# Kernel tuning notes

Measured on AMD Instinct MI355X. Metric: run time of the kernel, lower is better.

Reference implementation:

```python
import math
import jax, jax.numpy as jnp
import numpy as np

S, H, D = 2048, 16, 128

def setup_inputs() -> dict:
    key = jax.random.key(0)
    kq, kk, kv = jax.random.split(key, 3)
    Q = jax.random.normal(kq, (S, H, D), dtype=jnp.float32)
    K = jax.random.normal(kk, (S, H, D), dtype=jnp.float32)
    V = jax.random.normal(kv, (S, H, D), dtype=jnp.float32)
    return {"Q": Q, "K": K, "V": V}

def reference(Q, K, V):
    s, h, d = Q.shape
    # scores[i,h,j] = sum_d Q[i,h,d] * K[j,h,d]  (torch einsum 'ijk,kjl->ijl' with K.T)
    scores = jnp.einsum('ihd,jhd->ihj', Q, K) / np.float32(math.sqrt(d))
    # causal mask: y -= triu(inf, 1) broadcast over heads -> -inf above diagonal
    causal = jnp.triu(jnp.ones((s, s), dtype=bool), k=1)  # [S, S]
    scores = jnp.where(causal[:, None, :], -jnp.inf, scores)
    attn = jax.nn.softmax(scores, axis=2)  # softmax over keys (dim 2)
    # out[i,h,d] = sum_j attn[i,h,j] * V[j,h,d]
    return jnp.einsum('ihj,jhd->ihd', attn, V)
```

## Files before the change

kernel.cpp:

```cpp
#include <hip/hip_runtime.h>
#include <hip/hip_bf16.h>

#define S_LEN 2048
#define NH 16
#define HD 128
#define KBLK 64
#define SM_BOUND 14.0f

typedef short short8 __attribute__((ext_vector_type(8)));
typedef float f32x4 __attribute__((ext_vector_type(4)));

__device__ __forceinline__ ushort f2bf(float f) {
  union { float f; unsigned u; } v; v.f = f;
  unsigned u = v.u;
  return (ushort)((u + 0x7fffu + ((u >> 16) & 1u)) >> 16);
}

#define GLDS(gp, lp)                                                      \
  __builtin_amdgcn_global_load_lds(                                       \
      (const __attribute__((address_space(1))) void*)(gp),                \
      (__attribute__((address_space(3))) void*)(lp), 16, 0, 0)

__global__ __launch_bounds__(256)
void prep(const float* __restrict__ Kg, const float* __restrict__ Vg,
          ushort* __restrict__ Kb, ushort* __restrict__ Vb) {
  __shared__ ushort lt[64 * HD];
  const int tid = threadIdx.x;
  const int h = blockIdx.x & 15;
  const int j0 = (blockIdx.x >> 4) * 64;

#pragma unroll
  for (int it = 0; it < 8; ++it) {
    int flat = it * 256 + tid;
    int r = flat >> 5, d4 = (flat & 31) * 4;
    float4 v = *(const float4*)(Kg + ((size_t)(j0 + r) * NH + h) * HD + d4);
    ushort4 b;
    b.x = f2bf(v.x); b.y = f2bf(v.y); b.z = f2bf(v.z); b.w = f2bf(v.w);
    *(ushort4*)(Kb + ((size_t)h * S_LEN + j0 + r) * HD + d4) = b;
  }
#pragma unroll
  for (int it = 0; it < 8; ++it) {
    int flat = it * 256 + tid;
    int r = flat >> 5, d4 = (flat & 31) * 4;
    float4 v = *(const float4*)(Vg + ((size_t)(j0 + r) * NH + h) * HD + d4);
    ushort4 b;
    b.x = f2bf(v.x); b.y = f2bf(v.y); b.z = f2bf(v.z); b.w = f2bf(v.w);
    *(ushort4*)(&lt[r * 128 + (d4 ^ ((r & 7) << 3))]) = b;
  }
  __syncthreads();
  const int d = tid >> 1, half = tid & 1;
  ushort vals[32];
#pragma unroll
  for (int j = 0; j < 32; ++j) {
    int jjj = half * 32 + j;
    vals[j] = lt[jjj * 128 + (d ^ ((jjj & 7) << 3))];
  }
  ushort* dst = Vb + ((size_t)h * HD + d) * S_LEN + j0 + half * 32;
#pragma unroll
  for (int q = 0; q < 4; ++q) {
    short8 w;
#pragma unroll
    for (int e = 0; e < 8; ++e) w[e] = (short)vals[q * 8 + e];
    *(short8*)(dst + q * 8) = w;
  }
}

__global__ __launch_bounds__(512, 2)
void attn_fwd6(const float* __restrict__ Qg, const ushort* __restrict__ Kb,
               const ushort* __restrict__ Vb, float* __restrict__ Og) {
  __shared__ ushort lds_k[3][KBLK * HD];
  __shared__ ushort lds_vt[3][HD * KBLK];
  __shared__ ushort lds_p[64 * 64];
  __shared__ float  lsc[2][4][2][16];

  const int tid = threadIdx.x;
  const int l   = tid & 63;
  const int wv  = tid >> 6;
  const int qf  = wv >> 2;
  const int kh  = wv & 3;
  const int dh  = wv & 3;
  const int lr  = l & 15;
  const int lg  = l >> 4;

  const int bid = blockIdx.x;
  const int h   = bid & 15;
  const int jj  = bid >> 4;
  const int qtA = 31 - jj;
  const int qbA = qtA * 64, qbB = jj * 64;

  const ushort* khp = Kb + (size_t)h * S_LEN * HD;
  const ushort* vhp = Vb + (size_t)h * HD * S_LEN;

  const int b0 = tid, b1 = 512 + tid;
  const int r0 = b0 >> 4, r1 = b1 >> 4;
  const int koff0 = r0 * 128 + (((b0 & 15) ^ (r0 & 7)) << 3);
  const int koff1 = r1 * 128 + (((b1 & 15) ^ (r1 & 7)) << 3);
  const int dd0 = b0 >> 3, dd1 = b1 >> 3;
  const int voff0 = dd0 * S_LEN + (((b0 & 7) ^ (dd0 & 7)) << 3);
  const int voff1 = dd1 * S_LEN + (((b1 & 7) ^ (dd1 & 7)) << 3);

  auto stage = [&](int buf, int kc) {
    const ushort* kbase = khp + (size_t)kc * (KBLK * HD);
    GLDS(kbase + koff0, &lds_k[buf][tid * 8]);
    GLDS(kbase + koff1, &lds_k[buf][4096 + tid * 8]);
    const ushort* vbase = vhp + (size_t)kc * KBLK;
    GLDS(vbase + voff0, &lds_vt[buf][tid * 8]);
    GLDS(vbase + voff1, &lds_vt[buf][4096 + tid * 8]);
  };

  const float scale = 0.08838834764831845f;
  short8 qfrA[2][4], qfrB[2][4];
  auto loadQ = [&](short8 (&dst)[2][4], int qb) {
#pragma unroll
    for (int qc = 0; qc < 2; ++qc) {
      const float* qsrc = Qg + ((size_t)(qb + qf * 32 + qc * 16 + lr) * NH + h) * HD;
#pragma unroll
      for (int dk = 0; dk < 4; ++dk) {
        float4 a = *(const float4*)(qsrc + dk * 32 + lg * 8);
        float4 b2 = *(const float4*)(qsrc + dk * 32 + lg * 8 + 4);
        short8 f;
        f[0] = (short)f2bf(a.x * scale);  f[1] = (short)f2bf(a.y * scale);
        f[2] = (short)f2bf(a.z * scale);  f[3] = (short)f2bf(a.w * scale);
        f[4] = (short)f2bf(b2.x * scale); f[5] = (short)f2bf(b2.y * scale);
        f[6] = (short)f2bf(b2.z * scale); f[7] = (short)f2bf(b2.w * scale);
        dst[qc][dk] = f;
      }
    }
  };
  loadQ(qfrA, qbA);
  loadQ(qfrB, qbB);

  f32x4 oacc[2][2];
#pragma unroll
  for (int qc = 0; qc < 2; ++qc)
#pragma unroll
    for (int dt = 0; dt < 2; ++dt) oacc[qc][dt] = (f32x4){0.f, 0.f, 0.f, 0.f};
  float l_run[2] = {0.f, 0.f};

  auto epilogue = [&](int qb) {
    float t0 = l_run[0], t1 = l_run[1];
    t0 += __shfl_xor(t0, 16, 64); t0 += __shfl_xor(t0, 32, 64);
    t1 += __shfl_xor(t1, 16, 64); t1 += __shfl_xor(t1, 32, 64);
    if (lg == 0) { lsc[qf][kh][0][lr] = t0; lsc[qf][kh][1][lr] = t1; }
    __syncthreads();
    float inv[2][4];
#pragma unroll
    for (int qc = 0; qc < 2; ++qc)
#pragma unroll
      for (int i = 0; i < 4; ++i) {
        int q15 = lg * 4 + i;
        float sl = (lsc[qf][0][qc][q15] + lsc[qf][1][qc][q15]) +
                   (lsc[qf][2][qc][q15] + lsc[qf][3][qc][q15]);
        inv[qc][i] = 1.0f / sl;
      }
#pragma unroll
    for (int qc = 0; qc < 2; ++qc)
#pragma unroll
      for (int dt = 0; dt < 2; ++dt)
#pragma unroll
        for (int i = 0; i < 4; ++i) {
          int qg = qb + qf * 32 + qc * 16 + lg * 4 + i;
          Og[((size_t)qg * NH + h) * HD + dh * 32 + dt * 16 + lr] =
              oacc[qc][dt][i] * inv[qc][i];
        }
  };

  stage(0, 0);
  stage(1, 1);

  for (int g = 0; g < 33; ++g) {
    if (g == 32) { asm volatile("s_waitcnt vmcnt(0)" ::: "memory"); }
    else         { asm volatile("s_waitcnt vmcnt(4)" ::: "memory"); }
    asm volatile("s_barrier" ::: "memory");
    if (g + 2 < 33) {
      int t = g + 2;
      stage(t % 3, (t <= qtA) ? t : (t - qtA - 1));
    }
    const int bI = g % 3;
    const ushort* lk = lds_k[bI];
    const ushort* lv = lds_vt[bI];
    const bool tB = (g > qtA);
    const int kc = tB ? (g - qtA - 1) : g;
    const int qb = tB ? qbB : qbA;

    f32x4 s0 = (f32x4){0.f, 0.f, 0.f, 0.f};
    f32x4 s1 = (f32x4){0.f, 0.f, 0.f, 0.f};
    const int krow = kh * 16 + lr;
    __builtin_amdgcn_s_setprio(1);
    if (!tB) {
#pragma unroll
      for (int dk = 0; dk < 4; ++dk) {
        short8 kf = *(const short8*)&lk[krow * 128 + ((dk * 32 + lg * 8) ^ ((lr & 7) << 3))];
        s0 = __builtin_amdgcn_mfma_f32_16x16x32_bf16(kf, qfrA[0][dk], s0, 0, 0, 0);
        s1 = __builtin_amdgcn_mfma_f32_16x16x32_bf16(kf, qfrA[1][dk], s1, 0, 0, 0);
      }
    } else {
#pragma unroll
      for (int dk = 0; dk < 4; ++dk) {
        short8 kf = *(const short8*)&lk[krow * 128 + ((dk * 32 + lg * 8) ^ ((lr & 7) << 3))];
        s0 = __builtin_amdgcn_mfma_f32_16x16x32_bf16(kf, qfrB[0][dk], s0, 0, 0, 0);
        s1 = __builtin_amdgcn_mfma_f32_16x16x32_bf16(kf, qfrB[1][dk], s1, 0, 0, 0);
      }
    }
    __builtin_amdgcn_s_setprio(0);

    float p0[4], p1[4];
    if (g == qtA || g == 32) {
      const int qg0 = qb + qf * 32 + lr;
#pragma unroll
      for (int i = 0; i < 4; ++i) {
        int kg = kc * 64 + kh * 16 + lg * 4 + i;
        float e0 = __expf(s0[i] - SM_BOUND);
        float e1 = __expf(s1[i] - SM_BOUND);
        p0[i] = (kg > qg0) ? 0.f : e0;
        p1[i] = (kg > qg0 + 16) ? 0.f : e1;
      }
    } else {
#pragma unroll
      for (int i = 0; i < 4; ++i) {
        p0[i] = __expf(s0[i] - SM_BOUND);
        p1[i] = __expf(s1[i] - SM_BOUND);
      }
    }
    l_run[0] += (p0[0] + p0[1]) + (p0[2] + p0[3]);
    l_run[1] += (p1[0] + p1[1]) + (p1[2] + p1[3]);

    {
      int q0 = qf * 32 + lr;
      int q1 = q0 + 16;
      unsigned w;
      asm("v_cvt_pk_bf16_f32 %0, %1, %2" : "=v"(w) : "v"(p0[0]), "v"(p0[1]));
      *(unsigned*)&lds_p[q0 * 64 + ((kh * 16 + lg * 4 + 0) ^ ((q0 & 7) << 3))] = w;
      asm("v_cvt_pk_bf16_f32 %0, %1, %2" : "=v"(w) : "v"(p0[2]), "v"(p0[3]));
      *(unsigned*)&lds_p[q0 * 64 + ((kh * 16 + lg * 4 + 2) ^ ((q0 & 7) << 3))] = w;
      asm("v_cvt_pk_bf16_f32 %0, %1, %2" : "=v"(w) : "v"(p1[0]), "v"(p1[1]));
      *(unsigned*)&lds_p[q1 * 64 + ((kh * 16 + lg * 4 + 0) ^ ((q1 & 7) << 3))] = w;
      asm("v_cvt_pk_bf16_f32 %0, %1, %2" : "=v"(w) : "v"(p1[2]), "v"(p1[3]));
      *(unsigned*)&lds_p[q1 * 64 + ((kh * 16 + lg * 4 + 2) ^ ((q1 & 7) << 3))] = w;
    }
    asm volatile("s_waitcnt lgkmcnt(0)" ::: "memory");
    asm volatile("s_barrier" ::: "memory");
    __builtin_amdgcn_sched_barrier(0);

    short8 pa0[2], pa1[2];
    {
      int q0 = qf * 32 + lr;
      int q1 = q0 + 16;
      pa0[0] = *(const short8*)&lds_p[q0 * 64 + ((lg * 8) ^ ((q0 & 7) << 3))];
      pa0[1] = *(const short8*)&lds_p[q0 * 64 + ((32 + lg * 8) ^ ((q0 & 7) << 3))];
      pa1[0] = *(const short8*)&lds_p[q1 * 64 + ((lg * 8) ^ ((q1 & 7) << 3))];
      pa1[1] = *(const short8*)&lds_p[q1 * 64 + ((32 + lg * 8) ^ ((q1 & 7) << 3))];
    }
    __builtin_amdgcn_s_setprio(1);
#pragma unroll
    for (int dt = 0; dt < 2; ++dt) {
      int d = dh * 32 + dt * 16 + lr;
#pragma unroll
      for (int ks = 0; ks < 2; ++ks) {
        short8 vf = *(const short8*)&lv[d * 64 + ((ks * 32 + lg * 8) ^ ((d & 7) << 3))];
        oacc[0][dt] = __builtin_amdgcn_mfma_f32_16x16x32_bf16(pa0[ks], vf, oacc[0][dt], 0, 0, 0);
        oacc[1][dt] = __builtin_amdgcn_mfma_f32_16x16x32_bf16(pa1[ks], vf, oacc[1][dt], 0, 0, 0);
      }
    }
    __builtin_amdgcn_s_setprio(0);

    if (g == qtA) {
      epilogue(qbA);
#pragma unroll
      for (int qc = 0; qc < 2; ++qc)
#pragma unroll
        for (int dt = 0; dt < 2; ++dt) oacc[qc][dt] = (f32x4){0.f, 0.f, 0.f, 0.f};
      l_run[0] = 0.f; l_run[1] = 0.f;
    }
  }
  epilogue(qbB);
}

__global__ __launch_bounds__(256, 2)
void attn_fwd_fb(const float* __restrict__ Qg, const float* __restrict__ Kg,
                 const float* __restrict__ Vg, float* __restrict__ Og) {
  __shared__ ushort lds_k[KBLK * HD];
  __shared__ ushort lds_vt[HD * KBLK];
  __shared__ ushort lds_p[4][16 * KBLK];

  const int tid = threadIdx.x;
  const int l  = tid & 63;
  const int wv = tid >> 6;
  const int lr = l & 15;
  const int lg = l >> 4;

  const int bid = blockIdx.x;
  const int h  = bid & 15;
  const int qi = bid >> 4;
  const int qt = (qi < 16) ? (31 - 2 * qi) : (2 * (qi - 16));
  const int qbase = qt * 64;

  short8 qf[4];
  {
    const float* qsrc = Qg + ((size_t)(qbase + wv * 16 + lr) * NH + h) * HD;
#pragma unroll
    for (int dk = 0; dk < 4; ++dk) {
      float4 a = *(const float4*)(qsrc + dk * 32 + lg * 8);
      float4 b = *(const float4*)(qsrc + dk * 32 + lg * 8 + 4);
      short8 f;
      f[0] = (short)f2bf(a.x); f[1] = (short)f2bf(a.y);
      f[2] = (short)f2bf(a.z); f[3] = (short)f2bf(a.w);
      f[4] = (short)f2bf(b.x); f[5] = (short)f2bf(b.y);
      f[6] = (short)f2bf(b.z); f[7] = (short)f2bf(b.w);
      qf[dk] = f;
    }
  }

  f32x4 oacc[8];
#pragma unroll
  for (int dt = 0; dt < 8; ++dt) oacc[dt] = (f32x4){0.f, 0.f, 0.f, 0.f};
  float l_run[4] = {0.f, 0.f, 0.f, 0.f};

  const float scale = 0.08838834764831845f;
  const int nch = qt + 1;

  for (int c = 0; c < nch; ++c) {
    const int k0 = c * KBLK;
    __syncthreads();
#pragma unroll
    for (int it = 0; it < 8; ++it) {
      int flat = (it * 256 + tid) * 4;
      int r = flat >> 7, d = flat & 127;
      float4 v = *(const float4*)(Kg + ((size_t)(k0 + r) * NH + h) * HD + d);
      int idx = (r * 128 + d) ^ ((r & 7) << 3);
      ushort4 b4;
      b4.x = f2bf(v.x); b4.y = f2bf(v.y); b4.z = f2bf(v.z); b4.w = f2bf(v.w);
      *(ushort4*)&lds_k[idx] = b4;
    }
#pragma unroll
    for (int it = 0; it < 8; ++it) {
      int d0 = wv * 32 + it * 4;
      float4 v = *(const float4*)(Vg + ((size_t)(k0 + l) * NH + h) * HD + d0);
      lds_vt[((d0 + 0) * 64 + l) ^ (((d0 + 0) & 7) << 3)] = f2bf(v.x);
      lds_vt[((d0 + 1) * 64 + l) ^ (((d0 + 1) & 7) << 3)] = f2bf(v.y);
      lds_vt[((d0 + 2) * 64 + l) ^ (((d0 + 2) & 7) << 3)] = f2bf(v.z);
      lds_vt[((d0 + 3) * 64 + l) ^ (((d0 + 3) & 7) << 3)] = f2bf(v.w);
    }
    __syncthreads();

    f32x4 sacc[4];
#pragma unroll
    for (int kc = 0; kc < 4; ++kc) {
      sacc[kc] = (f32x4){0.f, 0.f, 0.f, 0.f};
#pragma unroll
      for (int dk = 0; dk < 4; ++dk) {
        int row = kc * 16 + lr;
        int idx = (row * 128 + dk * 32 + lg * 8) ^ ((row & 7) << 3);
        short8 kf = *(const short8*)&lds_k[idx];
        sacc[kc] = __builtin_amdgcn_mfma_f32_16x16x32_bf16(qf[dk], kf, sacc[kc], 0, 0, 0);
      }
    }

    float p[4][4];
    if (c == qt) {
#pragma unroll
      for (int i = 0; i < 4; ++i) {
        int qg = qbase + wv * 16 + lg * 4 + i;
#pragma unroll
        for (int kc = 0; kc < 4; ++kc) {
          float e = __expf(sacc[kc][i] * scale - SM_BOUND);
          p[kc][i] = (k0 + kc * 16 + lr > qg) ? 0.f : e;
        }
      }
    } else {
#pragma unroll
      for (int i = 0; i < 4; ++i)
#pragma unroll
        for (int kc = 0; kc < 4; ++kc)
          p[kc][i] = __expf(sacc[kc][i] * scale - SM_BOUND);
    }
#pragma unroll
    for (int i = 0; i < 4; ++i)
      l_run[i] += (p[0][i] + p[1][i]) + (p[2][i] + p[3][i]);

#pragma unroll
    for (int kc = 0; kc < 4; ++kc)
#pragma unroll
      for (int i = 0; i < 4; ++i) {
        int row = lg * 4 + i, col = kc * 16 + lr;
        lds_p[wv][(row * 64 + col) ^ ((row & 7) << 3)] = f2bf(p[kc][i]);
      }
    asm volatile("s_waitcnt lgkmcnt(0)" ::: "memory");
    __builtin_amdgcn_sched_barrier(0);

    short8 pa[2];
#pragma unroll
    for (int ks = 0; ks < 2; ++ks) {
      int idx = (lr * 64 + ks * 32 + lg * 8) ^ ((lr & 7) << 3);
      pa[ks] = *(const short8*)&lds_p[wv][idx];
    }

#pragma unroll
    for (int dt = 0; dt < 8; ++dt) {
#pragma unroll
      for (int ks = 0; ks < 2; ++ks) {
        int d = dt * 16 + lr;
        int idx = (d * 64 + ks * 32 + lg * 8) ^ ((d & 7) << 3);
        short8 vf = *(const short8*)&lds_vt[idx];
        oacc[dt] = __builtin_amdgcn_mfma_f32_16x16x32_bf16(pa[ks], vf, oacc[dt], 0, 0, 0);
      }
    }
  }

#pragma unroll
  for (int mk = 1; mk <= 8; mk <<= 1)
#pragma unroll
    for (int i = 0; i < 4; ++i)
      l_run[i] += __shfl_xor(l_run[i], mk, 64);
  float inv[4];
#pragma unroll
  for (int i = 0; i < 4; ++i) inv[i] = 1.0f / l_run[i];
#pragma unroll
  for (int dt = 0; dt < 8; ++dt)
#pragma unroll
    for (int i = 0; i < 4; ++i) {
      int qg = qbase + wv * 16 + lg * 4 + i;
      Og[((size_t)qg * NH + h) * HD + dt * 16 + lr] = oacc[dt][i] * inv[i];
    }
}

extern "C" void kernel_launch(void* const* d_in, const int* in_sizes, int n_in,
                              void* d_out, int out_size, void* d_ws, size_t ws_size,
                              hipStream_t stream) {
  (void)in_sizes; (void)n_in; (void)out_size;
  const float* Q = (const float*)d_in[0];
  const float* K = (const float*)d_in[1];
  const float* V = (const float*)d_in[2];
  float* O = (float*)d_out;

  const size_t elems = (size_t)S_LEN * NH * HD;
  const size_t need = 2 * elems * sizeof(ushort);
  if (ws_size >= need) {
    ushort* Kb = (ushort*)d_ws;
    ushort* Vb = Kb + elems;
    prep<<<dim3(512), dim3(256), 0, stream>>>(K, V, Kb, Vb);
    attn_fwd6<<<dim3(256), dim3(512), 0, stream>>>(Q, Kb, Vb, O);
  } else {
    attn_fwd_fb<<<dim3(512), dim3(256), 0, stream>>>(Q, K, V, O);
  }
}
```

Before: 64.36 us.

## Compute transposed S=K·Q^T so P stays in registers for PV MFMA

Adds an attention kernel that computes scores transposed (K rows times Q), so each lane's exp'd probabilities can feed a 16x16x16 bf16 MFMA for the PV product directly from registers. This avoids staging P through LDS. Each wave now covers a key slice with all 128 output dims. Partial output accumulators are then reduced across the four key-split waves in LDS during the epilogue, which adds barriers and more accumulator registers. The old kernel is kept as a fallback when the 16x16x16 MFMA builtin is unavailable.

```diff
diff --git a/kernel.cpp b/kernel.cpp
--- a/kernel.cpp
+++ b/kernel.cpp
@@ -8,7 +8,15 @@
 #define SM_BOUND 14.0f
 
 typedef short short8 __attribute__((ext_vector_type(8)));
+typedef short short4v __attribute__((ext_vector_type(4)));
 typedef float f32x4 __attribute__((ext_vector_type(4)));
+
+#if __has_builtin(__builtin_amdgcn_mfma_f32_16x16x16bf16_1k)
+#define HAVE_MFMA16 1
+#define MFMA16(a, b, c) __builtin_amdgcn_mfma_f32_16x16x16bf16_1k(a, b, c, 0, 0, 0)
+#else
+#define HAVE_MFMA16 0
+#endif
 
 __device__ __forceinline__ ushort f2bf(float f) {
   union { float f; unsigned u; } v; v.f = f;
@@ -65,8 +73,239 @@
   }
 }
 
+#if HAVE_MFMA16
 __global__ __launch_bounds__(512, 2)
-void attn_fwd6(const float* __restrict__ Qg, const ushort* __restrict__ Kb,
+void attn_main(const float* __restrict__ Qg, const ushort* __restrict__ Kb,
+               const ushort* __restrict__ Vb, float* __restrict__ Og) {
+  __shared__ ushort lds_k[3][KBLK * HD];
+  __shared__ ushort lds_vt[3][HD * KBLK];
+  __shared__ float  osc[2][4096];
+  __shared__ float  lsc[2][4][2][16];
+
+  const int tid = threadIdx.x;
+  const int l   = tid & 63;
+  const int wv  = tid >> 6;
+  const int qf  = wv >> 2;
+  const int kh  = wv & 3;
+  const int lr  = l & 15;
+  const int lg  = l >> 4;
+
+  const int bid = blockIdx.x;
+  const int h   = bid & 15;
+  const int jj  = bid >> 4;
+  const int qtA = 31 - jj;
+  const int qbA = qtA * 64, qbB = jj * 64;
+
+  const ushort* khp = Kb + (size_t)h * S_LEN * HD;
+  const ushort* vhp = Vb + (size_t)h * HD * S_LEN;
+
+  const int b0 = tid, b1 = 512 + tid;
+  const int r0 = b0 >> 4, r1 = b1 >> 4;
+  const int koff0 = r0 * 128 + (((b0 & 15) ^ (r0 & 7)) << 3);
+  const int koff1 = r1 * 128 + (((b1 & 15) ^ (r1 & 7)) << 3);
+  const int dd0 = b0 >> 3, dd1 = b1 >> 3;
+  const int voff0 = dd0 * S_LEN + (((b0 & 7) ^ (dd0 & 7)) << 3);
+  const int voff1 = dd1 * S_LEN + (((b1 & 7) ^ (dd1 & 7)) << 3);
+
+  auto stage = [&](int buf, int kc) {
+    const ushort* kbase = khp + (size_t)kc * (KBLK * HD);
+    GLDS(kbase + koff0, &lds_k[buf][tid * 8]);
+    GLDS(kbase + koff1, &lds_k[buf][4096 + tid * 8]);
+    const ushort* vbase = vhp + (size_t)kc * KBLK;
+    GLDS(vbase + voff0, &lds_vt[buf][tid * 8]);
+    GLDS(vbase + voff1, &lds_vt[buf][4096 + tid * 8]);
+  };
+
+  const float scale = 0.08838834764831845f;
+  short8 qfrA[2][4], qfrB[2][4];
+  auto loadQ = [&](short8 (&dst)[2][4], int qb) {
+#pragma unroll
+    for (int qc = 0; qc < 2; ++qc) {
+      const float* qsrc = Qg + ((size_t)(qb + qf * 32 + qc * 16 + lr) * NH + h) * HD;
+#pragma unroll
+      for (int dk = 0; dk < 4; ++dk) {
+        float4 a = *(const float4*)(qsrc + dk * 32 + lg * 8);
+        float4 b2 = *(const float4*)(qsrc + dk * 32 + lg * 8 + 4);
+        short8 f;
+        f[0] = (short)f2bf(a.x * scale);  f[1] = (short)f2bf(a.y * scale);
+        f[2] = (short)f2bf(a.z * scale);  f[3] = (short)f2bf(a.w * scale);
+        f[4] = (short)f2bf(b2.x * scale); f[5] = (short)f2bf(b2.y * scale);
+        f[6] = (short)f2bf(b2.z * scale); f[7] = (short)f2bf(b2.w * scale);
+        dst[qc][dk] = f;
+      }
+    }
+  };
+  loadQ(qfrA, qbA);
+  loadQ(qfrB, qbB);
+
+  f32x4 oaccT[2][8];
+#pragma unroll
+  for (int qc = 0; qc < 2; ++qc)
+#pragma unroll
+    for (int dt = 0; dt < 8; ++dt) oaccT[qc][dt] = (f32x4){0.f, 0.f, 0.f, 0.f};
+  float l_run[2] = {0.f, 0.f};
+
+  auto epilogue = [&](int qb) {
+    float t0 = l_run[0], t1 = l_run[1];
+    t0 += __shfl_xor(t0, 16, 64); t0 += __shfl_xor(t0, 32, 64);
+    t1 += __shfl_xor(t1, 16, 64); t1 += __shfl_xor(t1, 32, 64);
+    if (lg == 0) { lsc[qf][kh][0][lr] = t0; lsc[qf][kh][1][lr] = t1; }
+    if (kh == 0) {
+#pragma unroll
+      for (int qc = 0; qc < 2; ++qc)
+#pragma unroll
+        for (int dt = 0; dt < 8; ++dt) {
+          int q = qc * 16 + lr;
+          int du = (((dt * 4 + lg) ^ (q & 7)) << 2);
+          *(f32x4*)&osc[qf][q * 128 + du] = oaccT[qc][dt];
+        }
+    }
+    __syncthreads();
+    if (kh == 1) {
+#pragma unroll
+      for (int qc = 0; qc < 2; ++qc)
+#pragma unroll
+        for (int dt = 0; dt < 8; ++dt) {
+          int q = qc * 16 + lr;
+          int du = (((dt * 4 + lg) ^ (q & 7)) << 2);
+          f32x4 v = *(const f32x4*)&osc[qf][q * 128 + du];
+          v += oaccT[qc][dt];
+          *(f32x4*)&osc[qf][q * 128 + du] = v;
+        }
+    }
+    __syncthreads();
+    if (kh == 2) {
+#pragma unroll
+      for (int qc = 0; qc < 2; ++qc)
+#pragma unroll
+        for (int dt = 0; dt < 8; ++dt) {
+          int q = qc * 16 + lr;
+          int du = (((dt * 4 + lg) ^ (q & 7)) << 2);
+          f32x4 v = *(const f32x4*)&osc[qf][q * 128 + du];
+          v += oaccT[qc][dt];
+          *(f32x4*)&osc[qf][q * 128 + du] = v;
+        }
+    }
+    __syncthreads();
+    if (kh == 3) {
+      float inv[2];
+#pragma unroll
+      for (int qc = 0; qc < 2; ++qc)
+        inv[qc] = 1.0f / ((lsc[qf][0][qc][lr] + lsc[qf][1][qc][lr]) +
+                          (lsc[qf][2][qc][lr] + lsc[qf][3][qc][lr]));
+#pragma unroll
+      for (int qc = 0; qc < 2; ++qc)
+#pragma unroll
+        for (int dt = 0; dt < 8; ++dt) {
+          int q = qc * 16 + lr;
+          int du = (((dt * 4 + lg) ^ (q & 7)) << 2);
+          f32x4 v = *(const f32x4*)&osc[qf][q * 128 + du];
+          v += oaccT[qc][dt];
+          int qg = qb + qf * 32 + q;
+          float4 o;
+          o.x = v[0] * inv[qc]; o.y = v[1] * inv[qc];
+          o.z = v[2] * inv[qc]; o.w = v[3] * inv[qc];
+          *(float4*)(Og + ((size_t)qg * NH + h) * HD + dt * 16 + lg * 4) = o;
+        }
+    }
+  };
+
+  stage(0, 0);
+  stage(1, 1);
+
+  for (int g = 0; g < 33; ++g) {
+    if (g == 32) { asm volatile("s_waitcnt vmcnt(0)" ::: "memory"); }
+    else         { asm volatile("s_waitcnt vmcnt(4)" ::: "memory"); }
+    asm volatile("s_barrier" ::: "memory");
+    if (g + 2 < 33) {
+      int t = g + 2;
+      stage(t % 3, (t <= qtA) ? t : (t - qtA - 1));
+    }
+    const int bI = g % 3;
+    const ushort* lk = lds_k[bI];
+    const ushort* lv = lds_vt[bI];
+    const bool tB = (g > qtA);
+    const int kc = tB ? (g - qtA - 1) : g;
+    const int qb = tB ? qbB : qbA;
+
+    f32x4 s0 = (f32x4){0.f, 0.f, 0.f, 0.f};
+    f32x4 s1 = (f32x4){0.f, 0.f, 0.f, 0.f};
+    const int krow = kh * 16 + lr;
+    __builtin_amdgcn_s_setprio(1);
+    if (!tB) {
+#pragma unroll
+      for (int dk = 0; dk < 4; ++dk) {
+        short8 kf = *(const short8*)&lk[krow * 128 + ((dk * 32 + lg * 8) ^ ((lr & 7) << 3))];
+        s0 = __builtin_amdgcn_mfma_f32_16x16x32_bf16(kf, qfrA[0][dk], s0, 0, 0, 0);
+        s1 = __builtin_amdgcn_mfma_f32_16x16x32_bf16(kf, qfrA[1][dk], s1, 0, 0, 0);
+      }
+    } else {
+#pragma unroll
+      for (int dk = 0; dk < 4; ++dk) {
+        short8 kf = *(const short8*)&lk[krow * 128 + ((dk * 32 + lg * 8) ^ ((lr & 7) << 3))];
+        s0 = __builtin_amdgcn_mfma_f32_16x16x32_bf16(kf, qfrB[0][dk], s0, 0, 0, 0);
+        s1 = __builtin_amdgcn_mfma_f32_16x16x32_bf16(kf, qfrB[1][dk], s1, 0, 0, 0);
+      }
+    }
+    __builtin_amdgcn_s_setprio(0);
+
+    float p0[4], p1[4];
+    if (g == qtA || g == 32) {
+      const int qg0 = qb + qf * 32 + lr;
+#pragma unroll
+      for (int i = 0; i < 4; ++i) {
+        int kg = kc * 64 + kh * 16 + lg * 4 + i;
+        float e0 = __expf(s0[i] - SM_BOUND);
+        float e1 = __expf(s1[i] - SM_BOUND);
+        p0[i] = (kg > qg0) ? 0.f : e0;
+        p1[i] = (kg > qg0 + 16) ? 0.f : e1;
+      }
+    } else {
+#pragma unroll
+      for (int i = 0; i < 4; ++i) {
+        p0[i] = __expf(s0[i] - SM_BOUND);
+        p1[i] = __expf(s1[i] - SM_BOUND);
+      }
+    }
+    l_run[0] += (p0[0] + p0[1]) + (p0[2] + p0[3]);
+    l_run[1] += (p1[0] + p1[1]) + (p1[2] + p1[3]);
+
+    short4v pb0, pb1;
+    {
+      union { unsigned u[2]; short4v v; } c0, c1;
+      asm("v_cvt_pk_bf16_f32 %0, %1, %2" : "=v"(c0.u[0]) : "v"(p0[0]), "v"(p0[1]));
+      asm("v_cvt_pk_bf16_f32 %0, %1, %2" : "=v"(c0.u[1]) : "v"(p0[2]), "v"(p0[3]));
+      asm("v_cvt_pk_bf16_f32 %0, %1, %2" : "=v"(c1.u[0]) : "v"(p1[0]), "v"(p1[1]));
+      asm("v_cvt_pk_bf16_f32 %0, %1, %2" : "=v"(c1.u[1]) : "v"(p1[2]), "v"(p1[3]));
+      pb0 = c0.v; pb1 = c1.v;
+    }
+
+    __builtin_amdgcn_s_setprio(1);
+#pragma unroll
+    for (int dt = 0; dt < 8; ++dt) {
+      int d = dt * 16 + lr;
+      short4v va = *(const short4v*)&lv[d * 64 + ((kh * 16 + lg * 4) ^ ((d & 7) << 3))];
+      oaccT[0][dt] = MFMA16(va, pb0, oaccT[0][dt]);
+      oaccT[1][dt] = MFMA16(va, pb1, oaccT[1][dt]);
+    }
+    __builtin_amdgcn_s_setprio(0);
+
+    if (g == qtA) {
+      epilogue(qbA);
+#pragma unroll
+      for (int qc = 0; qc < 2; ++qc)
+#pragma unroll
+        for (int dt = 0; dt < 8; ++dt) oaccT[qc][dt] = (f32x4){0.f, 0.f, 0.f, 0.f};
+      l_run[0] = 0.f; l_run[1] = 0.f;
+    }
+  }
+  epilogue(qbB);
+}
+
+#else
+
+__global__ __launch_bounds__(512, 2)
+void attn_main(const float* __restrict__ Qg, const ushort* __restrict__ Kb,
                const ushort* __restrict__ Vb, float* __restrict__ Og) {
   __shared__ ushort lds_k[3][KBLK * HD];
   __shared__ ushort lds_vt[3][HD * KBLK];
@@ -275,6 +514,7 @@
   }
   epilogue(qbB);
 }
+#endif
 
 __global__ __launch_bounds__(256, 2)
 void attn_fwd_fb(const float* __restrict__ Qg, const float* __restrict__ Kg,
@@ -439,7 +679,7 @@
     ushort* Kb = (ushort*)d_ws;
     ushort* Vb = Kb + elems;
     prep<<<dim3(512), dim3(256), 0, stream>>>(K, V, Kb, Vb);
-    attn_fwd6<<<dim3(256), dim3(512), 0, stream>>>(Q, Kb, Vb, O);
+    attn_main<<<dim3(256), dim3(512), 0, stream>>>(Q, Kb, Vb, O);
   } else {
     attn_fwd_fb<<<dim3(512), dim3(256), 0, stream>>>(Q, K, V, O);
   }
```

New measurement: 67.02 us. 4.1% more time.

## Split each paired causal attention block across two workgroups with partial-sum combine

Applied to the files above, without the earlier changes.

Replaces the single 256-block kernel, where each block processed a paired long and short query tile, with a 512-block kernel. Each pair of blocks splits the 33 key chunks about evenly (16 and 17): one block does half of the long tile, the other finishes it and also does the short tile. The long tile's partial outputs and row sums go to workspace and a new combine kernel merges them. Inside the kernel, P stays in registers and feeds 16x16x16 MFMAs with each wave covering all 128 head dimensions, dropping the P round-trip through LDS. The trade-off is a cross-wave LDS reduction in the epilogue, an extra kernel launch, more workspace traffic, and the fixed max-bound softmax is unchanged.

```diff
diff --git a/kernel.cpp b/kernel.cpp
--- a/kernel.cpp
+++ b/kernel.cpp
@@ -8,7 +8,11 @@
 #define SM_BOUND 14.0f
 
 typedef short short8 __attribute__((ext_vector_type(8)));
+typedef short short4v __attribute__((ext_vector_type(4)));
 typedef float f32x4 __attribute__((ext_vector_type(4)));
+
+#define MFMA32(a, b, c) __builtin_amdgcn_mfma_f32_16x16x32_bf16(a, b, c, 0, 0, 0)
+#define MFMA16(a, b, c) __builtin_amdgcn_mfma_f32_16x16x16bf16_1k(a, b, c, 0, 0, 0)
 
 __device__ __forceinline__ ushort f2bf(float f) {
   union { float f; unsigned u; } v; v.f = f;
@@ -65,12 +69,13 @@
   }
 }
 
-__global__ __launch_bounds__(512, 2)
-void attn_fwd6(const float* __restrict__ Qg, const ushort* __restrict__ Kb,
-               const ushort* __restrict__ Vb, float* __restrict__ Og) {
-  __shared__ ushort lds_k[3][KBLK * HD];
-  __shared__ ushort lds_vt[3][HD * KBLK];
-  __shared__ ushort lds_p[64 * 64];
+__global__ __launch_bounds__(512, 4)
+void attn_split2(const float* __restrict__ Qg, const ushort* __restrict__ Kb,
+                 const ushort* __restrict__ Vb, float* __restrict__ Og,
+                 float* __restrict__ Opart, float* __restrict__ lpart) {
+  __shared__ ushort lds_k[2][KBLK * HD];
+  __shared__ ushort lds_vt[2][HD * KBLK];
+  __shared__ float  osc[16 * 128];
   __shared__ float  lsc[2][4][2][16];
 
   const int tid = threadIdx.x;
@@ -78,39 +83,47 @@
   const int wv  = tid >> 6;
   const int qf  = wv >> 2;
   const int kh  = wv & 3;
-  const int dh  = wv & 3;
   const int lr  = l & 15;
   const int lg  = l >> 4;
 
   const int bid = blockIdx.x;
-  const int h   = bid & 15;
-  const int jj  = bid >> 4;
-  const int qtA = 31 - jj;
-  const int qbA = qtA * 64, qbB = jj * 64;
+  const int w    = bid >> 3;
+  const int h    = ((bid & 7) << 1) + (w >> 5);
+  const int r5v  = w & 31;
+  const int jj   = r5v >> 1;
+  const int role = r5v & 1;
+  const int qtA  = 31 - jj;
+  const int qbA  = qtA << 6, qbB = jj << 6;
+  const int pid  = h * 16 + jj;
+  const int nA   = role ? (16 - jj) : 16;
+  const int nch  = role ? 17 : 16;
+  const int kcA0 = role ? 16 : 0;
 
   const ushort* khp = Kb + (size_t)h * S_LEN * HD;
   const ushort* vhp = Vb + (size_t)h * HD * S_LEN;
 
-  const int b0 = tid, b1 = 512 + tid;
-  const int r0 = b0 >> 4, r1 = b1 >> 4;
-  const int koff0 = r0 * 128 + (((b0 & 15) ^ (r0 & 7)) << 3);
-  const int koff1 = r1 * 128 + (((b1 & 15) ^ (r1 & 7)) << 3);
-  const int dd0 = b0 >> 3, dd1 = b1 >> 3;
-  const int voff0 = dd0 * S_LEN + (((b0 & 7) ^ (dd0 & 7)) << 3);
-  const int voff1 = dd1 * S_LEN + (((b1 & 7) ^ (dd1 & 7)) << 3);
-
+  int koff[2], voff[2];
+#pragma unroll
+  for (int i = 0; i < 2; ++i) {
+    int Dg = i * 512 + tid;
+    int r = Dg >> 4, c = Dg & 15;
+    koff[i] = r * 128 + ((c ^ (r & 7)) << 3);
+    int d = Dg >> 3, gp = Dg & 7;
+    voff[i] = d * S_LEN + (((gp - (d & 7)) & 7) << 3);
+  }
   auto stage = [&](int buf, int kc) {
     const ushort* kbase = khp + (size_t)kc * (KBLK * HD);
-    GLDS(kbase + koff0, &lds_k[buf][tid * 8]);
-    GLDS(kbase + koff1, &lds_k[buf][4096 + tid * 8]);
+    GLDS(kbase + koff[0], &lds_k[buf][tid * 8]);
+    GLDS(kbase + koff[1], &lds_k[buf][4096 + tid * 8]);
     const ushort* vbase = vhp + (size_t)kc * KBLK;
-    GLDS(vbase + voff0, &lds_vt[buf][tid * 8]);
-    GLDS(vbase + voff1, &lds_vt[buf][4096 + tid * 8]);
+    GLDS(vbase + voff[0], &lds_vt[buf][tid * 8]);
+    GLDS(vbase + voff[1], &lds_vt[buf][4096 + tid * 8]);
   };
+  auto kc_of = [&](int g) { return (g < nA) ? (kcA0 + g) : (g - nA); };
 
   const float scale = 0.08838834764831845f;
-  short8 qfrA[2][4], qfrB[2][4];
-  auto loadQ = [&](short8 (&dst)[2][4], int qb) {
+  short8 qfr[2][4];
+  auto loadQ = [&](int qb) {
 #pragma unroll
     for (int qc = 0; qc < 2; ++qc) {
       const float* qsrc = Qg + ((size_t)(qb + qf * 32 + qc * 16 + lr) * NH + h) * HD;
@@ -123,89 +136,120 @@
         f[2] = (short)f2bf(a.z * scale);  f[3] = (short)f2bf(a.w * scale);
         f[4] = (short)f2bf(b2.x * scale); f[5] = (short)f2bf(b2.y * scale);
         f[6] = (short)f2bf(b2.z * scale); f[7] = (short)f2bf(b2.w * scale);
-        dst[qc][dk] = f;
+        qfr[qc][dk] = f;
       }
     }
   };
-  loadQ(qfrA, qbA);
-  loadQ(qfrB, qbB);
-
-  f32x4 oacc[2][2];
+  loadQ(qbA);
+
+  f32x4 oaccT[2][8];
 #pragma unroll
   for (int qc = 0; qc < 2; ++qc)
 #pragma unroll
-    for (int dt = 0; dt < 2; ++dt) oacc[qc][dt] = (f32x4){0.f, 0.f, 0.f, 0.f};
+    for (int dt = 0; dt < 8; ++dt) oaccT[qc][dt] = (f32x4){0.f, 0.f, 0.f, 0.f};
   float l_run[2] = {0.f, 0.f};
 
-  auto epilogue = [&](int qb) {
+  auto epilogue = [&](int mode, int qb, int slot) {
     float t0 = l_run[0], t1 = l_run[1];
     t0 += __shfl_xor(t0, 16, 64); t0 += __shfl_xor(t0, 32, 64);
     t1 += __shfl_xor(t1, 16, 64); t1 += __shfl_xor(t1, 32, 64);
     if (lg == 0) { lsc[qf][kh][0][lr] = t0; lsc[qf][kh][1][lr] = t1; }
-    __syncthreads();
-    float inv[2][4];
-#pragma unroll
-    for (int qc = 0; qc < 2; ++qc)
-#pragma unroll
-      for (int i = 0; i < 4; ++i) {
-        int q15 = lg * 4 + i;
-        float sl = (lsc[qf][0][qc][q15] + lsc[qf][1][qc][q15]) +
-                   (lsc[qf][2][qc][q15] + lsc[qf][3][qc][q15]);
-        inv[qc][i] = 1.0f / sl;
-      }
-#pragma unroll
-    for (int qc = 0; qc < 2; ++qc)
-#pragma unroll
-      for (int dt = 0; dt < 2; ++dt)
-#pragma unroll
-        for (int i = 0; i < 4; ++i) {
-          int qg = qb + qf * 32 + qc * 16 + lg * 4 + i;
-          Og[((size_t)qg * NH + h) * HD + dh * 32 + dt * 16 + lr] =
-              oacc[qc][dt][i] * inv[qc][i];
+    asm volatile("s_waitcnt lgkmcnt(0)" ::: "memory");
+    asm volatile("s_barrier" ::: "memory");
+    const size_t pid2 = (size_t)(pid * 2 + slot);
+#pragma unroll
+    for (int qfp = 0; qfp < 2; ++qfp)
+#pragma unroll
+      for (int qcp = 0; qcp < 2; ++qcp) {
+        if (qf == qfp && kh == 0) {
+#pragma unroll
+          for (int dt = 0; dt < 8; ++dt)
+            *(f32x4*)&osc[lr * 128 + (((dt * 4 + lg) ^ (lr & 7)) << 2)] = oaccT[qcp][dt];
         }
+        asm volatile("s_waitcnt lgkmcnt(0)" ::: "memory");
+        asm volatile("s_barrier" ::: "memory");
+        if (qf == qfp && kh == 1) {
+#pragma unroll
+          for (int dt = 0; dt < 8; ++dt) {
+            f32x4 v = *(const f32x4*)&osc[lr * 128 + (((dt * 4 + lg) ^ (lr & 7)) << 2)];
+            v += oaccT[qcp][dt];
+            *(f32x4*)&osc[lr * 128 + (((dt * 4 + lg) ^ (lr & 7)) << 2)] = v;
+          }
+        }
+        asm volatile("s_waitcnt lgkmcnt(0)" ::: "memory");
+        asm volatile("s_barrier" ::: "memory");
+        if (qf == qfp && kh == 2) {
+#pragma unroll
+          for (int dt = 0; dt < 8; ++dt) {
+            f32x4 v = *(const f32x4*)&osc[lr * 128 + (((dt * 4 + lg) ^ (lr & 7)) << 2)];
+            v += oaccT[qcp][dt];
+            *(f32x4*)&osc[lr * 128 + (((dt * 4 + lg) ^ (lr & 7)) << 2)] = v;
+          }
+        }
+        asm volatile("s_waitcnt lgkmcnt(0)" ::: "memory");
+        asm volatile("s_barrier" ::: "memory");
+        if (qf == qfp && kh == 3) {
+          float lsum = (lsc[qfp][0][qcp][lr] + lsc[qfp][1][qcp][lr]) +
+                       (lsc[qfp][2][qcp][lr] + lsc[qfp][3][qcp][lr]);
+          int qrow = qfp * 32 + qcp * 16 + lr;
+          if (mode == 0) {
+            if (lg == 0) lpart[pid2 * 64 + qrow] = lsum;
+            float* dst = Opart + pid2 * 8192 + (size_t)qrow * 128;
+#pragma unroll
+            for (int dt = 0; dt < 8; ++dt) {
+              f32x4 v = *(const f32x4*)&osc[lr * 128 + (((dt * 4 + lg) ^ (lr & 7)) << 2)];
+              v += oaccT[qcp][dt];
+              float4 o; o.x = v[0]; o.y = v[1]; o.z = v[2]; o.w = v[3];
+              *(float4*)(dst + dt * 16 + lg * 4) = o;
+            }
+          } else {
+            float inv = 1.0f / lsum;
+            int qg = qb + qrow;
+#pragma unroll
+            for (int dt = 0; dt < 8; ++dt) {
+              f32x4 v = *(const f32x4*)&osc[lr * 128 + (((dt * 4 + lg) ^ (lr & 7)) << 2)];
+              v += oaccT[qcp][dt];
+              float4 o;
+              o.x = v[0] * inv; o.y = v[1] * inv; o.z = v[2] * inv; o.w = v[3] * inv;
+              *(float4*)(Og + ((size_t)qg * NH + h) * HD + dt * 16 + lg * 4) = o;
+            }
+          }
+        }
+        asm volatile("s_waitcnt lgkmcnt(0)" ::: "memory");
+        asm volatile("s_barrier" ::: "memory");
+      }
   };
 
-  stage(0, 0);
-  stage(1, 1);
-
-  for (int g = 0; g < 33; ++g) {
-    if (g == 32) { asm volatile("s_waitcnt vmcnt(0)" ::: "memory"); }
-    else         { asm volatile("s_waitcnt vmcnt(4)" ::: "memory"); }
+  stage(0, kc_of(0));
+  stage(1, kc_of(1));
+
+  for (int g = 0; g < nch; ++g) {
+    if (g + 1 < nch) { asm volatile("s_waitcnt vmcnt(4)" ::: "memory"); }
+    else             { asm volatile("s_waitcnt vmcnt(0)" ::: "memory"); }
     asm volatile("s_barrier" ::: "memory");
-    if (g + 2 < 33) {
-      int t = g + 2;
-      stage(t % 3, (t <= qtA) ? t : (t - qtA - 1));
-    }
-    const int bI = g % 3;
-    const ushort* lk = lds_k[bI];
-    const ushort* lv = lds_vt[bI];
-    const bool tB = (g > qtA);
-    const int kc = tB ? (g - qtA - 1) : g;
+
+    const int b = g & 1;
+    const ushort* lk = lds_k[b];
+    const ushort* lv = lds_vt[b];
+    const bool tB = (g >= nA);
+    const int kc = kc_of(g);
     const int qb = tB ? qbB : qbA;
+    const bool diag = ((kc << 6) == qb);
 
     f32x4 s0 = (f32x4){0.f, 0.f, 0.f, 0.f};
     f32x4 s1 = (f32x4){0.f, 0.f, 0.f, 0.f};
     const int krow = kh * 16 + lr;
     __builtin_amdgcn_s_setprio(1);
-    if (!tB) {
-#pragma unroll
-      for (int dk = 0; dk < 4; ++dk) {
-        short8 kf = *(const short8*)&lk[krow * 128 + ((dk * 32 + lg * 8) ^ ((lr & 7) << 3))];
-        s0 = __builtin_amdgcn_mfma_f32_16x16x32_bf16(kf, qfrA[0][dk], s0, 0, 0, 0);
-        s1 = __builtin_amdgcn_mfma_f32_16x16x32_bf16(kf, qfrA[1][dk], s1, 0, 0, 0);
-      }
-    } else {
-#pragma unroll
-      for (int dk = 0; dk < 4; ++dk) {
-        short8 kf = *(const short8*)&lk[krow * 128 + ((dk * 32 + lg * 8) ^ ((lr & 7) << 3))];
-        s0 = __builtin_amdgcn_mfma_f32_16x16x32_bf16(kf, qfrB[0][dk], s0, 0, 0, 0);
-        s1 = __builtin_amdgcn_mfma_f32_16x16x32_bf16(kf, qfrB[1][dk], s1, 0, 0, 0);
-      }
+#pragma unroll
+    for (int dk = 0; dk < 4; ++dk) {
+      short8 kf = *(const short8*)&lk[krow * 128 + ((dk * 32 + lg * 8) ^ ((krow & 7) << 3))];
+      s0 = MFMA32(kf, qfr[0][dk], s0);
+      s1 = MFMA32(kf, qfr[1][dk], s1);
     }
     __builtin_amdgcn_s_setprio(0);
 
     float p0[4], p1[4];
-    if (g == qtA || g == 32) {
+    if (diag) {
       const int qg0 = qb + qf * 32 + lr;
 #pragma unroll
       for (int i = 0; i < 4; ++i) {
@@ -225,55 +269,69 @@
     l_run[0] += (p0[0] + p0[1]) + (p0[2] + p0[3]);
     l_run[1] += (p1[0] + p1[1]) + (p1[2] + p1[3]);
 
+    short4v pb0, pb1;
     {
-      int q0 = qf * 32 + lr;
-      int q1 = q0 + 16;
-      unsigned w;
-      asm("v_cvt_pk_bf16_f32 %0, %1, %2" : "=v"(w) : "v"(p0[0]), "v"(p0[1]));
-      *(unsigned*)&lds_p[q0 * 64 + ((kh * 16 + lg * 4 + 0) ^ ((q0 & 7) << 3))] = w;
-      asm("v_cvt_pk_bf16_f32 %0, %1, %2" : "=v"(w) : "v"(p0[2]), "v"(p0[3]));
-      *(unsigned*)&lds_p[q0 * 64 + ((kh * 16 + lg * 4 + 2) ^ ((q0 & 7) << 3))] = w;
-      asm("v_cvt_pk_bf16_f32 %0, %1, %2" : "=v"(w) : "v"(p1[0]), "v"(p1[1]));
-      *(unsigned*)&lds_p[q1 * 64 + ((kh * 16 + lg * 4 + 0) ^ ((q1 & 7) << 3))] = w;
-      asm("v_cvt_pk_bf16_f32 %0, %1, %2" : "=v"(w) : "v"(p1[2]), "v"(p1[3]));
-      *(unsigned*)&lds_p[q1 * 64 + ((kh * 16 + lg * 4 + 2) ^ ((q1 & 7) << 3))] = w;
-    }
-    asm volatile("s_waitcnt lgkmcnt(0)" ::: "memory");
+      union { unsigned u[2]; short4v v; } c0, c1;
+      asm("v_cvt_pk_bf16_f32 %0, %1, %2" : "=v"(c0.u[0]) : "v"(p0[0]), "v"(p0[1]));
+      asm("v_cvt_pk_bf16_f32 %0, %1, %2" : "=v"(c0.u[1]) : "v"(p0[2]), "v"(p0[3]));
+      asm("v_cvt_pk_bf16_f32 %0, %1, %2" : "=v"(c1.u[0]) : "v"(p1[0]), "v"(p1[1]));
+      asm("v_cvt_pk_bf16_f32 %0, %1, %2" : "=v"(c1.u[1]) : "v"(p1[2]), "v"(p1[3]));
+      pb0 = c0.v; pb1 = c1.v;
+    }
+
+    __builtin_amdgcn_s_setprio(1);
+#pragma unroll
+    for (int dt = 0; dt < 8; ++dt) {
+      int d = dt * 16 + lr;
+      int col = ((kh * 16 + lg * 4) + ((d & 7) << 3)) & 63;
+      short4v va = *(const short4v*)&lv[d * 64 + col];
+      oaccT[0][dt] = MFMA16(va, pb0, oaccT[0][dt]);
+      oaccT[1][dt] = MFMA16(va, pb1, oaccT[1][dt]);
+    }
+    __builtin_amdgcn_s_setprio(0);
+
     asm volatile("s_barrier" ::: "memory");
-    __builtin_amdgcn_sched_barrier(0);
-
-    short8 pa0[2], pa1[2];
-    {
-      int q0 = qf * 32 + lr;
-      int q1 = q0 + 16;
-      pa0[0] = *(const short8*)&lds_p[q0 * 64 + ((lg * 8) ^ ((q0 & 7) << 3))];
-      pa0[1] = *(const short8*)&lds_p[q0 * 64 + ((32 + lg * 8) ^ ((q0 & 7) << 3))];
-      pa1[0] = *(const short8*)&lds_p[q1 * 64 + ((lg * 8) ^ ((q1 & 7) << 3))];
-      pa1[1] = *(const short8*)&lds_p[q1 * 64 + ((32 + lg * 8) ^ ((q1 & 7) << 3))];
-    }
-    __builtin_amdgcn_s_setprio(1);
-#pragma unroll
-    for (int dt = 0; dt < 2; ++dt) {
-      int d = dh * 32 + dt * 16 + lr;
-#pragma unroll
-      for (int ks = 0; ks < 2; ++ks) {
-        short8 vf = *(const short8*)&lv[d * 64 + ((ks * 32 + lg * 8) ^ ((d & 7) << 3))];
-        oacc[0][dt] = __builtin_amdgcn_mfma_f32_16x16x32_bf16(pa0[ks], vf, oacc[0][dt], 0, 0, 0);
-        oacc[1][dt] = __builtin_amdgcn_mfma_f32_16x16x32_bf16(pa1[ks], vf, oacc[1][dt], 0, 0, 0);
-      }
-    }
-    __builtin_amdgcn_s_setprio(0);
-
-    if (g == qtA) {
-      epilogue(qbA);
+    if (g + 2 < nch) stage(b, kc_of(g + 2));
+
+    if (role && g == nA - 1) {
+      epilogue(0, qbA, 1);
 #pragma unroll
       for (int qc = 0; qc < 2; ++qc)
 #pragma unroll
-        for (int dt = 0; dt < 2; ++dt) oacc[qc][dt] = (f32x4){0.f, 0.f, 0.f, 0.f};
+        for (int dt = 0; dt < 8; ++dt) oaccT[qc][dt] = (f32x4){0.f, 0.f, 0.f, 0.f};
       l_run[0] = 0.f; l_run[1] = 0.f;
-    }
-  }
-  epilogue(qbB);
+      loadQ(qbB);
+      asm volatile("s_waitcnt vmcnt(0)" ::: "memory");
+    }
+  }
+
+  if (role) epilogue(1, qbB, 0);
+  else      epilogue(0, qbA, 0);
+}
+
+__global__ __launch_bounds__(256)
+void combine(const float* __restrict__ Opart, const float* __restrict__ lpart,
+             float* __restrict__ Og) {
+  const int pid = blockIdx.x;
+  const int h = pid >> 4, jj = pid & 15;
+  const int qbase = (31 - jj) * 64;
+  const int t = threadIdx.x;
+  const int q = t >> 2, d0 = (t & 3) * 32;
+  const float* p0 = Opart + (size_t)(pid * 2) * 8192 + q * 128 + d0;
+  const float* p1 = p0 + 8192;
+  const float lsum = lpart[(size_t)(pid * 2) * 64 + q] +
+                     lpart[(size_t)(pid * 2 + 1) * 64 + q];
+  const float inv = 1.0f / lsum;
+  float* og = Og + ((size_t)(qbase + q) * NH + h) * HD + d0;
+#pragma unroll
+  for (int e = 0; e < 32; e += 4) {
+    float4 a = *(const float4*)(p0 + e);
+    float4 b = *(const float4*)(p1 + e);
+    float4 o;
+    o.x = (a.x + b.x) * inv; o.y = (a.y + b.y) * inv;
+    o.z = (a.z + b.z) * inv; o.w = (a.w + b.w) * inv;
+    *(float4*)(og + e) = o;
+  }
 }
 
 __global__ __launch_bounds__(256, 2)
@@ -352,7 +410,7 @@
         int row = kc * 16 + lr;
         int idx = (row * 128 + dk * 32 + lg * 8) ^ ((row & 7) << 3);
         short8 kf = *(const short8*)&lds_k[idx];
-        sacc[kc] = __builtin_amdgcn_mfma_f32_16x16x32_bf16(qf[dk], kf, sacc[kc], 0, 0, 0);
+        sacc[kc] = MFMA32(qf[dk], kf, sacc[kc]);
       }
     }
 
@@ -402,7 +460,7 @@
         int d = dt * 16 + lr;
         int idx = (d * 64 + ks * 32 + lg * 8) ^ ((d & 7) << 3);
         short8 vf = *(const short8*)&lds_vt[idx];
-        oacc[dt] = __builtin_amdgcn_mfma_f32_16x16x32_bf16(pa[ks], vf, oacc[dt], 0, 0, 0);
+        oacc[dt] = MFMA32(pa[ks], vf, oacc[dt]);
       }
     }
   }
@@ -433,13 +491,20 @@
   const float* V = (const float*)d_in[2];
   float* O = (float*)d_out;
 
-  const size_t elems = (size_t)S_LEN * NH * HD;
-  const size_t need = 2 * elems * sizeof(ushort);
-  if (ws_size >= need) {
+  const size_t elems  = (size_t)S_LEN * NH * HD;
+  const size_t needKV = 2 * elems * sizeof(ushort);
+  const size_t oPartB = (size_t)256 * 2 * 8192 * 4;
+  const size_t lPartB = (size_t)256 * 2 * 64 * 4;
+  const size_t needSplit = needKV + oPartB + lPartB;
+
+  if (ws_size >= needSplit) {
     ushort* Kb = (ushort*)d_ws;
     ushort* Vb = Kb + elems;
+    float* Opart = (float*)((char*)d_ws + needKV);
+    float* lpart = (float*)((char*)d_ws + needKV + oPartB);
     prep<<<dim3(512), dim3(256), 0, stream>>>(K, V, Kb, Vb);
-    attn_fwd6<<<dim3(256), dim3(512), 0, stream>>>(Q, Kb, Vb, O);
+    attn_split2<<<dim3(512), dim3(512), 0, stream>>>(Q, Kb, Vb, O, Opart, lpart);
+    combine<<<dim3(256), dim3(256), 0, stream>>>(Opart, lpart, O);
   } else {
     attn_fwd_fb<<<dim3(512), dim3(256), 0, stream>>>(Q, K, V, O);
   }
```

Measured after the change: 101.8 us. 1.58x slower.
